# Kernel tuning notes

Measured on AMD Instinct MI355X. Metric: run time of the kernel, lower is better.

## Reference

```python
import jax, jax.numpy as jnp
import numpy as np

D, K, CIN, CD, COUT = 3, 16, 128, 32, 256
C = CIN + CD                  # 160 = C_in + C_delta after concat
DM = -(-COUT // C)            # depth_multiplier = ceil(C_out / C) = 2
N, I = 4, 2048                # batch, points per cloud; M = N*I = 8192


def _bn(x, g, b, eps=1e-5):
    # BatchNorm1d in training mode: biased batch statistics over dim 0
    mu = x.mean(0)
    v = x.var(0)
    return (x - mu) * jax.lax.rsqrt(v + eps) * g + b


def _knn(p, k):
    # knn_graph over ALL M points (wrapper passes no batch vector), loop=True
    d2 = jnp.sum(p * p, axis=1)
    dist = d2[:, None] + d2[None, :] - 2.0 * (p @ p.T)   # [M,M]
    _, idx = jax.lax.top_k(-dist, k)                     # [M,K], self first
    return idx


def _gconv(t, w, b, M):
    # grouped Conv1d(K, K*K, kernel=K, groups=K): t [M,K,K], w [K(cin), K(out/grp), K(tap)]
    return jnp.einsum('mcl,col->mco', t, w).reshape(M, K * K) + b


def _xconv(xf, pf, idx, w1a, b1a, g1a, be1a, w1b, b1b, g1b, be1b,
           w2, b2, g2a, be2a, wc2a, bc2a, g2b, be2b, wc2b, bc2b, g2c, be2c,
           wcd, bcd, wl, bl):
    M = pf.shape[0]
    rel = pf[idx] - pf[:, None, :]                       # [M,K,D] relative neighbor coords
    # mlp1: lift relative coords to C_delta features
    h = rel.reshape(M * K, D)
    h = _bn(jax.nn.elu(h @ w1a + b1a), g1a, be1a)
    h = _bn(jax.nn.elu(h @ w1b + b1b), g1b, be1b)
    x_star = jnp.concatenate([h.reshape(M, K, CD), xf[idx]], axis=-1)  # [M,K,C]
    x_star = x_star.transpose(0, 2, 1)                   # [M,C,K]
    # mlp2: learn KxK X-transformation from the K*D relative coords
    t = _bn(jax.nn.elu(rel.reshape(M, K * D) @ w2 + b2), g2a, be2a).reshape(M, K, K)
    t = _bn(jax.nn.elu(_gconv(t, wc2a, bc2a, M)), g2b, be2b).reshape(M, K, K)
    t = _bn(_gconv(t, wc2b, bc2b, M), g2c, be2c).reshape(M, K, K)
    xt = jnp.einsum('mck,mkj->mcj', x_star, t)           # [M,C,K] batched matmul
    # depthwise Conv1d(C, C*DM, K, groups=C) collapses K, then final Linear
    y = jnp.einsum('mcl,col->mco', xt, wcd).reshape(M, C * DM) + bcd
    return y @ wl + bl                                   # [M,COUT]


def setup_inputs() -> dict:
    key = jax.random.key(0)
    ks = jax.random.split(key, 16)
    r = lambda k, s: jax.random.normal(k, s, jnp.float32) * 0.1
    return dict(
        x=jax.random.normal(ks[0], (N, I, CIN), jnp.float32),
        pos=jax.random.normal(ks[1], (N, I, D), jnp.float32),
        w1a=r(ks[2], (D, CD)), b1a=r(ks[3], (CD,)), g1a=jnp.ones((CD,)), be1a=jnp.zeros((CD,)),
        w1b=r(ks[4], (CD, CD)), b1b=r(ks[5], (CD,)), g1b=jnp.ones((CD,)), be1b=jnp.zeros((CD,)),
        w2=r(ks[6], (D * K, K * K)), b2=r(ks[7], (K * K,)), g2a=jnp.ones((K * K,)), be2a=jnp.zeros((K * K,)),
        wc2a=r(ks[8], (K, K, K)), bc2a=r(ks[9], (K * K,)), g2b=jnp.ones((K * K,)), be2b=jnp.zeros((K * K,)),
        wc2b=r(ks[10], (K, K, K)), bc2b=r(ks[11], (K * K,)), g2c=jnp.ones((K * K,)), be2c=jnp.zeros((K * K,)),
        wcd=r(ks[12], (C, DM, K)), bcd=r(ks[13], (C * DM,)),
        wl=r(ks[14], (C * DM, COUT)), bl=r(ks[15], (COUT,)),
    )


def reference(x, pos, w1a, b1a, g1a, be1a, w1b, b1b, g1b, be1b,
              w2, b2, g2a, be2a, wc2a, bc2a, g2b, be2b, wc2b, bc2b, g2c, be2c,
              wcd, bcd, wl, bl):
    pf = pos.reshape(N * I, D)
    xf = x.reshape(N * I, CIN)
    idx = _knn(pf, K)
    out = _xconv(xf, pf, idx, w1a, b1a, g1a, be1a, w1b, b1b, g1b, be1b,
                 w2, b2, g2a, be2a, wc2a, bc2a, g2b, be2b, wc2b, bc2b, g2c, be2c,
                 wcd, bcd, wl, bl)
    return out.reshape(N, I, COUT)
```

## Files before the change

### kernel.cpp

```cpp
#include <hip/hip_runtime.h>
#include <math.h>

#define M_PTS 8192
#define MK    131072

__device__ __forceinline__ float elu(float v){ return v > 0.f ? v : __expf(v)-1.0f; }

__device__ __forceinline__ unsigned distkey(float4 c, float qx, float qy, float qz, float d2q){
  #pragma clang fp contract(off)
  float dot  = __builtin_fmaf(c.z, qz, __builtin_fmaf(c.y, qy, __builtin_fmaf(c.x, qx, 0.0f)));
  float A    = d2q + c.w;
  float B    = 2.0f * dot;
  float dist = A - B;
  unsigned u = __float_as_uint(dist);
  return u ^ ((unsigned)((int)u >> 31) | 0x80000000u);
}

__global__ __launch_bounds__(256) void knn_kernel(const float* __restrict__ pos,
                                                  int* __restrict__ nidx,
                                                  float* __restrict__ st){
  #pragma clang fp contract(off)
  __shared__ float4 cand[1024];
  __shared__ unsigned long long hits[4][64];
  int tid  = threadIdx.x;
  int lane = tid & 63;
  int wv   = tid >> 6;
  int q    = blockIdx.x*4 + wv;
  if (blockIdx.x == 0){
    for (int i = tid; i < 2048; i += 256) st[i] = 0.f;
  }
  float qx = pos[3*q], qy = pos[3*q+1], qz = pos[3*q+2];
  float d2q = (qx*qx + qy*qy) + qz*qz;

  unsigned ka[8];
  #pragma unroll
  for (int s=0;s<8;s++) ka[s] = 0xFFFFFFFFu;

  for (int base = 0; base < M_PTS; base += 1024){
    for (int t = tid; t < 1024; t += 256){
      int j = base + t;
      float x = pos[3*j], y = pos[3*j+1], z = pos[3*j+2];
      float d2v = (x*x + y*y) + z*z;
      cand[t] = make_float4(x,y,z,d2v);
    }
    __syncthreads();
    #pragma unroll
    for (int k=0; k<16; k++){
      unsigned v = distkey(cand[lane + k*64], qx, qy, qz, d2q);
      #pragma unroll
      for (int s=0;s<8;s++){
        unsigned mn = min(v, ka[s]);
        unsigned mx = max(v, ka[s]);
        ka[s] = mn; v = mx;
      }
    }
    __syncthreads();
  }

  unsigned thr = 0xFFFFFFFFu;
  for (int r=0; r<16; r++){
    unsigned mine = ka[0];
    unsigned best = mine;
    #pragma unroll
    for (int off=32; off>0; off>>=1){
      unsigned o = __shfl_xor(best, off, 64);
      best = min(best, o);
    }
    bool adv = (best == mine);
    #pragma unroll
    for (int s=0;s<7;s++) ka[s] = adv ? ka[s+1] : ka[s];
    ka[7] = adv ? 0xFFFFFFFFu : ka[7];
    thr = best;
  }

  int cnt = 0;
  for (int base = 0; base < M_PTS; base += 1024){
    for (int t = tid; t < 1024; t += 256){
      int j = base + t;
      float x = pos[3*j], y = pos[3*j+1], z = pos[3*j+2];
      float d2v = (x*x + y*y) + z*z;
      cand[t] = make_float4(x,y,z,d2v);
    }
    __syncthreads();
    #pragma unroll
    for (int k=0; k<16; k++){
      int j = base + lane + k*64;
      unsigned u = distkey(cand[lane + k*64], qx, qy, qz, d2q);
      bool hit = (u <= thr);
      unsigned long long m = __ballot(hit);
      if (hit){
        int slot = cnt + __popcll(m & ((1ull<<lane)-1ull));
        if (slot < 64) hits[wv][slot] = ((unsigned long long)u << 32) | (unsigned)j;
      }
      cnt += (int)__popcll(m);
    }
    __syncthreads();
  }

  int cc = min(cnt, 64);
  unsigned long long mine = (lane < cc) ? hits[wv][lane] : ~0ull;
  for (int r=0; r<16; r++){
    unsigned long long best = mine;
    #pragma unroll
    for (int off=32; off>0; off>>=1){
      unsigned long long o = __shfl_xor(best, off, 64);
      best = (o < best) ? o : best;
    }
    if (mine == best) mine = ~0ull;
    if (lane == 0) nidx[q*16 + r] = (int)(unsigned)best;
  }
}

#define COMPUTE_RELF_8()                                              \
  for (int f = tid; f < 8*48; f += 256){                              \
    int p = f/48, kd = f%48, k = kd/3, d = kd%3;                      \
    int j = nidx[(m0+p)*16 + k];                                      \
    relf[p][kd] = pos[3*j+d] - pos[3*(m0+p)+d];                       \
  }                                                                   \
  __syncthreads();

#define COMPUTE_T1_8(acc)                                             \
  _Pragma("unroll")                                                   \
  for (int p=0;p<8;p++) acc[p] = b2[tid];                             \
  for (int kk=0; kk<48; kk++){                                        \
    float w = w2[kk*256 + tid];                                       \
    _Pragma("unroll")                                                 \
    for (int p=0;p<8;p++) acc[p] += relf[p][kk]*w;                    \
  }

__global__ __launch_bounds__(256) void stats_a_kernel(const float* __restrict__ pos,
    const int* __restrict__ nidx,
    const float* __restrict__ w1a, const float* __restrict__ b1a,
    const float* __restrict__ w2,  const float* __restrict__ b2,
    float* __restrict__ tact,
    float* __restrict__ s1, float* __restrict__ s3){
  int tid = threadIdx.x;
  if (blockIdx.x < 512){
    __shared__ float relS[256][3];
    __shared__ float red[8][64];
    int r = blockIdx.x*256 + tid;
    int m = r >> 4;
    int j = nidx[r];
    relS[tid][0] = pos[3*j  ]-pos[3*m  ];
    relS[tid][1] = pos[3*j+1]-pos[3*m+1];
    relS[tid][2] = pos[3*j+2]-pos[3*m+2];
    __syncthreads();
    int c = tid & 31, g = tid >> 5;
    float w0=w1a[c], w1v=w1a[32+c], w2v=w1a[64+c], b=b1a[c];
    float s=0.f, q=0.f;
    for (int rr=g*32; rr<g*32+32; rr++){
      float h = elu(b + relS[rr][0]*w0 + relS[rr][1]*w1v + relS[rr][2]*w2v);
      s += h; q += h*h;
    }
    red[g][c]=s; red[g][32+c]=q;
    __syncthreads();
    if (tid < 64){
      float a=0.f;
      #pragma unroll
      for (int gg=0;gg<8;gg++) a += red[gg][tid];
      atomicAdd(&s1[tid], a);
    }
  } else {
    __shared__ float relf[8][48];
    int m0 = (blockIdx.x-512)*8;
    COMPUTE_RELF_8();
    float acc[8];
    COMPUTE_T1_8(acc);
    float s=0.f, q=0.f;
    #pragma unroll
    for (int p=0;p<8;p++){
      float v = elu(acc[p]);
      s += v; q += v*v;
      tact[(size_t)(m0+p)*256 + tid] = v;
    }
    atomicAdd(&s3[tid], s); atomicAdd(&s3[256+tid], q);
  }
}

__global__ __launch_bounds__(256) void stats_b_kernel(const float* __restrict__ pos,
    const int* __restrict__ nidx,
    const float* __restrict__ w1a, const float* __restrict__ b1a,
    const float* __restrict__ s1,  const float* __restrict__ g1a, const float* __restrict__ be1a,
    const float* __restrict__ w1b, const float* __restrict__ b1b,
    float* __restrict__ tact,
    const float* __restrict__ s3,  const float* __restrict__ g2a, const float* __restrict__ be2a,
    const float* __restrict__ wc2a,const float* __restrict__ bc2a,
    float* __restrict__ s2, float* __restrict__ s4){
  int tid = threadIdx.x;
  const float invMK = 1.f/(float)MK;
  const float invM  = 1.f/8192.f;
  if (blockIdx.x < 2048){
    __shared__ float xnS[64][33];
    __shared__ float red[8][64];
    __shared__ float muA[32], ivA[32];
    if (tid < 32){
      float mu  = s1[tid]*invMK;
      float var = s1[32+tid]*invMK - mu*mu;
      muA[tid] = mu; ivA[tid] = rsqrtf(var+1e-5f)*g1a[tid];
    }
    __syncthreads();
    {
      int rl = tid >> 2;
      int r  = blockIdx.x*64 + rl;
      int m = r >> 4;
      int j = nidx[r];
      float rx = pos[3*j]-pos[3*m], ry = pos[3*j+1]-pos[3*m+1], rz = pos[3*j+2]-pos[3*m+2];
      int c0 = (tid & 3)*8;
      #pragma unroll
      for (int u=0; u<8; u++){
        int cc = c0 + u;
        float h = elu(b1a[cc] + rx*w1a[cc] + ry*w1a[32+cc] + rz*w1a[64+cc]);
        xnS[rl][cc] = (h-muA[cc])*ivA[cc] + be1a[cc];
      }
    }
    __syncthreads();
    int o = tid & 31, g = tid >> 5;
    float wcol[32];
    #pragma unroll
    for (int cc=0;cc<32;cc++) wcol[cc] = w1b[cc*32+o];
    float bo = b1b[o], s=0.f, q=0.f;
    for (int rr=g*8; rr<g*8+8; rr++){
      float a = bo;
      #pragma unroll
      for (int cc=0;cc<32;cc++) a += xnS[rr][cc]*wcol[cc];
      float v = elu(a);
      s += v; q += v*v;
    }
    red[g][o]=s; red[g][32+o]=q;
    __syncthreads();
    if (tid < 64){
      float a=0.f;
      #pragma unroll
      for (int gg=0;gg<8;gg++) a += red[gg][tid];
      atomicAdd(&s2[tid], a);
    }
  } else {
    __shared__ float tn[8][256];
    int m0 = (blockIdx.x-2048)*8;
    float mu3  = s3[tid]*invM;
    float var3 = s3[256+tid]*invM - mu3*mu3;
    float i3   = rsqrtf(var3+1e-5f)*g2a[tid];
    float bb3  = be2a[tid];
    float tv[8];
    #pragma unroll
    for (int p=0;p<8;p++) tv[p] = tact[(size_t)(m0+p)*256 + tid];
    #pragma unroll
    for (int p=0;p<8;p++) tn[p][tid] = (tv[p]-mu3)*i3 + bb3;
    __syncthreads();
    int c = tid >> 4;
    float wreg[16];
    const float4* wv4 = (const float4*)(wc2a + tid*16);
    #pragma unroll
    for (int v=0; v<4; v++){ float4 f = wv4[v]; wreg[4*v]=f.x; wreg[4*v+1]=f.y; wreg[4*v+2]=f.z; wreg[4*v+3]=f.w; }
    float bias = bc2a[tid];
    float s=0.f, q=0.f;
    #pragma unroll
    for (int p=0;p<8;p++){
      float a2 = bias;
      #pragma unroll
      for (int l=0;l<16;l++) a2 += tn[p][c*16+l]*wreg[l];
      float v = elu(a2);
      s += v; q += v*v;
      tv[p] = v;
    }
    #pragma unroll
    for (int p=0;p<8;p++) tact[(size_t)(m0+p)*256 + tid] = tv[p];
    atomicAdd(&s4[tid], s); atomicAdd(&s4[256+tid], q);
  }
}

__global__ __launch_bounds__(256) void t3_stats_kernel(
    float* __restrict__ tact,
    const float* __restrict__ s4, const float* __restrict__ g2b, const float* __restrict__ be2b,
    const float* __restrict__ wc2b, const float* __restrict__ bc2b, float* __restrict__ s5){
  __shared__ float tn2[8][256];
  int m0 = blockIdx.x*8, tid = threadIdx.x;
  const float invM = 1.f/8192.f;
  float mu4  = s4[tid]*invM;
  float var4 = s4[256+tid]*invM - mu4*mu4;
  float i4   = rsqrtf(var4+1e-5f)*g2b[tid];
  float bb4  = be2b[tid];
  float tv[8];
  #pragma unroll
  for (int p=0;p<8;p++) tv[p] = tact[(size_t)(m0+p)*256 + tid];
  #pragma unroll
  for (int p=0;p<8;p++) tn2[p][tid] = (tv[p]-mu4)*i4 + bb4;
  __syncthreads();
  int c = tid >> 4;
  float w2reg[16];
  { const float4* wv4 = (const float4*)(wc2b + tid*16);
    #pragma unroll
    for (int v=0; v<4; v++){ float4 f = wv4[v]; w2reg[4*v]=f.x; w2reg[4*v+1]=f.y; w2reg[4*v+2]=f.z; w2reg[4*v+3]=f.w; } }
  float bias2 = bc2b[tid];
  float s=0.f, q=0.f;
  #pragma unroll
  for (int p=0;p<8;p++){
    float a3 = bias2;
    #pragma unroll
    for (int l=0;l<16;l++) a3 += tn2[p][c*16+l]*w2reg[l];
    s += a3; q += a3*a3;
    tv[p] = a3;
  }
  #pragma unroll
  for (int p=0;p<8;p++) tact[(size_t)(m0+p)*256 + tid] = tv[p];
  atomicAdd(&s5[tid], s); atomicAdd(&s5[256+tid], q);
}

#define PF 4
__global__ __launch_bounds__(256) void final_kernel(
    const float* __restrict__ x, const float* __restrict__ pos, const int* __restrict__ nidx,
    const float* __restrict__ w1a, const float* __restrict__ b1a,
    const float* __restrict__ g1a, const float* __restrict__ be1a,
    const float* __restrict__ w1b, const float* __restrict__ b1b,
    const float* __restrict__ g1b, const float* __restrict__ be1b,
    const float* __restrict__ g2c, const float* __restrict__ be2c,
    const float* __restrict__ wcd, const float* __restrict__ bcd,
    const float* __restrict__ wl,  const float* __restrict__ bl,
    const float* __restrict__ st,
    float* __restrict__ out){
  __shared__ float tA[PF][256];
  __shared__ float xs[PF*32*17];
  __shared__ float yy[PF][320];
  __shared__ int   sidx[PF*16];
  __shared__ float mu1[32], i1g[32], mu2[32], i2g[32];
  int tid = threadIdx.x;
  int m0  = blockIdx.x*PF;
  const float invMK = 1.f/(float)MK;
  const float invM  = 1.f/8192.f;

  if (tid < PF*16) sidx[tid] = nidx[m0*16 + tid];
  if (tid < 32){
    float mu  = st[tid]*invMK;
    float var = st[32+tid]*invMK - mu*mu;
    mu1[tid] = mu; i1g[tid] = rsqrtf(var+1e-5f)*g1a[tid];
    float mu_2  = st[64+tid]*invMK;
    float var_2 = st[96+tid]*invMK - mu_2*mu_2;
    mu2[tid] = mu_2; i2g[tid] = rsqrtf(var_2+1e-5f)*g1b[tid];
  }
  {
    float mu5 = st[1152+tid]*invM, var5 = st[1408+tid]*invM - mu5*mu5;
    float i5 = rsqrtf(var5+1e-5f)*g2c[tid], bb5 = be2c[tid];
    #pragma unroll
    for (int p=0;p<PF;p++){
      float v = out[(size_t)(m0+p)*256 + tid];
      tA[p][tid] = (v-mu5)*i5 + bb5;
    }
  }
  __syncthreads();

  {
    int row = tid >> 2;
    int p = row >> 4, k = row & 15;
    int q8 = (tid & 3)*8;
    int m = m0 + p;
    int j = sidx[p*16 + k];
    float rx = pos[3*j]-pos[3*m], ry = pos[3*j+1]-pos[3*m+1], rz = pos[3*j+2]-pos[3*m+2];
    float xn[32];
    #pragma unroll
    for (int cc=0; cc<32; cc++){
      float h = elu(b1a[cc] + rx*w1a[cc] + ry*w1a[32+cc] + rz*w1a[64+cc]);
      xn[cc] = (h-mu1[cc])*i1g[cc] + be1a[cc];
    }
    #pragma unroll
    for (int oo=0; oo<8; oo++){
      int o = q8 + oo;
      float a = b1b[o];
      #pragma unroll
      for (int cc=0; cc<32; cc++) a += xn[cc]*w1b[cc*32+o];
      float h2v = elu(a);
      xs[(p*32 + o)*17 + k] = (h2v-mu2[o])*i2g[o] + be1b[o];
    }
  }
  __syncthreads();

  for (int pair = tid; pair < PF*160; pair += 256){
    int p = pair / 160, cch = pair % 160;
    float av[16];
    if (cch < 32){
      #pragma unroll
      for (int k16=0;k16<16;k16++) av[k16] = xs[(p*32+cch)*17 + k16];
    } else {
      #pragma unroll
      for (int k16=0;k16<16;k16++) av[k16] = x[(size_t)sidx[p*16+k16]*128 + (cch-32)];
    }
    float xt[16];
    #pragma unroll
    for (int j16=0;j16<16;j16++) xt[j16]=0.f;
    #pragma unroll
    for (int k16=0;k16<16;k16++){
      float a = av[k16];
      #pragma unroll
      for (int j16=0;j16<16;j16++) xt[j16] += a*tA[p][k16*16+j16];
    }
    float y0 = bcd[cch*2], y1 = bcd[cch*2+1];
    #pragma unroll
    for (int l=0;l<16;l++){
      y0 += xt[l]*wcd[cch*32 + l];
      y1 += xt[l]*wcd[cch*32 + 16 + l];
    }
    yy[p][cch*2] = y0; yy[p][cch*2+1] = y1;
  }
  __syncthreads();

  float accO[PF];
  #pragma unroll
  for (int p=0;p<PF;p++) accO[p] = bl[tid];
  for (int q=0;q<320;q++){
    float w = wl[q*256 + tid];
    #pragma unroll
    for (int p=0;p<PF;p++) accO[p] += yy[p][q]*w;
  }
  #pragma unroll
  for (int p=0;p<PF;p++) out[(size_t)(m0+p)*256 + tid] = accO[p];
}

extern "C" void kernel_launch(void* const* d_in, const int* in_sizes, int n_in,
                              void* d_out, int out_size, void* d_ws, size_t ws_size,
                              hipStream_t stream){
  const float* x    = (const float*)d_in[0];
  const float* pos  = (const float*)d_in[1];
  const float* w1a  = (const float*)d_in[2];
  const float* b1a  = (const float*)d_in[3];
  const float* g1a  = (const float*)d_in[4];
  const float* be1a = (const float*)d_in[5];
  const float* w1b  = (const float*)d_in[6];
  const float* b1b  = (const float*)d_in[7];
  const float* g1b  = (const float*)d_in[8];
  const float* be1b = (const float*)d_in[9];
  const float* w2   = (const float*)d_in[10];
  const float* b2   = (const float*)d_in[11];
  const float* g2a  = (const float*)d_in[12];
  const float* be2a = (const float*)d_in[13];
  const float* wc2a = (const float*)d_in[14];
  const float* bc2a = (const float*)d_in[15];
  const float* g2b  = (const float*)d_in[16];
  const float* be2b = (const float*)d_in[17];
  const float* wc2b = (const float*)d_in[18];
  const float* bc2b = (const float*)d_in[19];
  const float* g2c  = (const float*)d_in[20];
  const float* be2c = (const float*)d_in[21];
  const float* wcd  = (const float*)d_in[22];
  const float* bcd  = (const float*)d_in[23];
  const float* wl   = (const float*)d_in[24];
  const float* bl   = (const float*)d_in[25];
  float* out = (float*)d_out;

  char* ws = (char*)d_ws;
  int*   nidx = (int*)(ws + 0);
  float* st   = (float*)(ws + 524288);
  float* s1 = st;
  float* s2 = st + 64;
  float* s3 = st + 128;
  float* s4 = st + 640;
  float* s5 = st + 1152;

  knn_kernel<<<2048,256,0,stream>>>(pos, nidx, st);
  stats_a_kernel<<<1536,256,0,stream>>>(pos, nidx, w1a, b1a, w2, b2, out, s1, s3);
  stats_b_kernel<<<3072,256,0,stream>>>(pos, nidx, w1a, b1a, s1, g1a, be1a, w1b, b1b,
                                        out, s3, g2a, be2a, wc2a, bc2a, s2, s4);
  t3_stats_kernel<<<1024,256,0,stream>>>(out, s4, g2b, be2b, wc2b, bc2b, s5);
  final_kernel<<<2048,256,0,stream>>>(x, pos, nidx,
                                      w1a, b1a, g1a, be1a, w1b, b1b, g1b, be1b,
                                      g2c, be2c, wcd, bcd, wl, bl, st, out);
}
```

Baseline: 392.3 us.

## Use bf16 MFMA for final linear layer and double points per block

```diff
diff --git a/kernel.cpp b/kernel.cpp
--- a/kernel.cpp
+++ b/kernel.cpp
@@ -4,7 +4,20 @@
 #define M_PTS 8192
 #define MK    131072
 
+typedef __attribute__((ext_vector_type(8))) short bf16x8;
+typedef __attribute__((ext_vector_type(4))) float f32x4;
+
 __device__ __forceinline__ float elu(float v){ return v > 0.f ? v : __expf(v)-1.0f; }
+
+__device__ __forceinline__ unsigned cvt_pk_bf16(float lo, float hi){
+  unsigned r;
+  asm("v_cvt_pk_bf16_f32 %0, %1, %2" : "=v"(r) : "v"(lo), "v"(hi));
+  return r;
+}
+__device__ __forceinline__ unsigned short f2bf(float v){
+  unsigned u = __float_as_uint(v);
+  return (unsigned short)((u + 0x7FFFu + ((u>>16)&1u)) >> 16);
+}
 
 __device__ __forceinline__ unsigned distkey(float4 c, float qx, float qy, float qz, float d2q){
   #pragma clang fp contract(off)
@@ -306,7 +319,7 @@
   atomicAdd(&s5[tid], s); atomicAdd(&s5[256+tid], q);
 }
 
-#define PF 4
+#define PF 8
 __global__ __launch_bounds__(256) void final_kernel(
     const float* __restrict__ x, const float* __restrict__ pos, const int* __restrict__ nidx,
     const float* __restrict__ w1a, const float* __restrict__ b1a,
@@ -319,8 +332,8 @@
     const float* __restrict__ st,
     float* __restrict__ out){
   __shared__ float tA[PF][256];
-  __shared__ float xs[PF*32*17];
-  __shared__ float yy[PF][320];
+  __shared__ unsigned short xs[PF*32*17];
+  __shared__ unsigned short yh[16][328];
   __shared__ int   sidx[PF*16];
   __shared__ float mu1[32], i1g[32], mu2[32], i2g[32];
   int tid = threadIdx.x;
@@ -338,6 +351,10 @@
     mu2[tid] = mu_2; i2g[tid] = rsqrtf(var_2+1e-5f)*g1b[tid];
   }
   {
+    unsigned short* yz = &yh[8][0];
+    for (int i = tid; i < 8*328; i += 256) yz[i] = 0;
+  }
+  {
     float mu5 = st[1152+tid]*invM, var5 = st[1408+tid]*invM - mu5*mu5;
     float i5 = rsqrtf(var5+1e-5f)*g2c[tid], bb5 = be2c[tid];
     #pragma unroll
@@ -348,12 +365,12 @@
   }
   __syncthreads();
 
-  {
-    int row = tid >> 2;
-    int p = row >> 4, k = row & 15;
+  for (int half = 0; half < 2; ++half){
+    int row = half*64 + (tid >> 2);
+    int p = row >> 4;
     int q8 = (tid & 3)*8;
     int m = m0 + p;
-    int j = sidx[p*16 + k];
+    int j = sidx[row];
     float rx = pos[3*j]-pos[3*m], ry = pos[3*j+1]-pos[3*m+1], rz = pos[3*j+2]-pos[3*m+2];
     float xn[32];
     #pragma unroll
@@ -361,6 +378,7 @@
       float h = elu(b1a[cc] + rx*w1a[cc] + ry*w1a[32+cc] + rz*w1a[64+cc]);
       xn[cc] = (h-mu1[cc])*i1g[cc] + be1a[cc];
     }
+    int k = row & 15;
     #pragma unroll
     for (int oo=0; oo<8; oo++){
       int o = q8 + oo;
@@ -368,7 +386,7 @@
       #pragma unroll
       for (int cc=0; cc<32; cc++) a += xn[cc]*w1b[cc*32+o];
       float h2v = elu(a);
-      xs[(p*32 + o)*17 + k] = (h2v-mu2[o])*i2g[o] + be1b[o];
+      xs[(p*32 + o)*17 + k] = f2bf((h2v-mu2[o])*i2g[o] + be1b[o]);
     }
   }
   __syncthreads();
@@ -378,7 +396,8 @@
     float av[16];
     if (cch < 32){
       #pragma unroll
-      for (int k16=0;k16<16;k16++) av[k16] = xs[(p*32+cch)*17 + k16];
+      for (int k16=0;k16<16;k16++)
+        av[k16] = __uint_as_float((unsigned)xs[(p*32+cch)*17 + k16] << 16);
     } else {
       #pragma unroll
       for (int k16=0;k16<16;k16++) av[k16] = x[(size_t)sidx[p*16+k16]*128 + (cch-32)];
@@ -398,20 +417,47 @@
       y0 += xt[l]*wcd[cch*32 + l];
       y1 += xt[l]*wcd[cch*32 + 16 + l];
     }
-    yy[p][cch*2] = y0; yy[p][cch*2+1] = y1;
+    *(unsigned*)&yh[p][cch*2] = cvt_pk_bf16(y0, y1);
   }
   __syncthreads();
 
-  float accO[PF];
-  #pragma unroll
-  for (int p=0;p<PF;p++) accO[p] = bl[tid];
-  for (int q=0;q<320;q++){
-    float w = wl[q*256 + tid];
-    #pragma unroll
-    for (int p=0;p<PF;p++) accO[p] += yy[p][q]*w;
-  }
-  #pragma unroll
-  for (int p=0;p<PF;p++) out[(size_t)(m0+p)*256 + tid] = accO[p];
+  {
+    int lane = tid & 63;
+    int wvi  = tid >> 6;
+    int lrow = lane & 15;
+    int lgrp = lane >> 4;
+    int colbase = wvi*64;
+    f32x4 acc[4];
+    #pragma unroll
+    for (int nt=0; nt<4; ++nt) acc[nt] = (f32x4){0.f,0.f,0.f,0.f};
+    for (int kt = 0; kt < 10; ++kt){
+      int k0 = kt*32 + lgrp*8;
+      bf16x8 ah = *(const bf16x8*)&yh[lrow][k0];
+      #pragma unroll
+      for (int nt = 0; nt < 4; ++nt){
+        int col = colbase + nt*16 + lrow;
+        const float* wp = wl + (size_t)k0*256 + col;
+        float w0=wp[0],    w1=wp[256],  w2=wp[512],  w3=wp[768];
+        float w4=wp[1024], w5=wp[1280], w6=wp[1536], w7=wp[1792];
+        union { bf16x8 v; unsigned u[4]; } bu;
+        bu.u[0] = cvt_pk_bf16(w0, w1);
+        bu.u[1] = cvt_pk_bf16(w2, w3);
+        bu.u[2] = cvt_pk_bf16(w4, w5);
+        bu.u[3] = cvt_pk_bf16(w6, w7);
+        acc[nt] = __builtin_amdgcn_mfma_f32_16x16x32_bf16(ah, bu.v, acc[nt], 0, 0, 0);
+      }
+    }
+    #pragma unroll
+    for (int nt=0; nt<4; ++nt){
+      int col = colbase + nt*16 + lrow;
+      float bv = bl[col];
+      #pragma unroll
+      for (int r=0;r<4;r++){
+        int orow = lgrp*4 + r;
+        if (orow < PF) out[(size_t)(m0+orow)*256 + col] = acc[nt][r] + bv;
+      }
+    }
+  }
 }
 
 extern "C" void kernel_launch(void* const* d_in, const int* in_sizes, int n_in,
@@ -459,7 +505,7 @@
   stats_b_kernel<<<3072,256,0,stream>>>(pos, nidx, w1a, b1a, s1, g1a, be1a, w1b, b1b,
                                         out, s3, g2a, be2a, wc2a, bc2a, s2, s4);
   t3_stats_kernel<<<1024,256,0,stream>>>(out, s4, g2b, be2b, wc2b, bc2b, s5);
-  final_kernel<<<2048,256,0,stream>>>(x, pos, nidx,
+  final_kernel<<<1024,256,0,stream>>>(x, pos, nidx,
                                       w1a, b1a, g1a, be1a, w1b, b1b, g1b, be1b,
                                       g2c, be2c, wcd, bcd, wl, bl, st, out);
 }
```

New measurement: 404.0 us. 3.0% more time.

## Split final linear into separate bf16 MFMA GEMM kernel via packed staging

Applied to the files above, without the earlier changes.

```diff
diff --git a/kernel.cpp b/kernel.cpp
--- a/kernel.cpp
+++ b/kernel.cpp
@@ -4,7 +4,16 @@
 #define M_PTS 8192
 #define MK    131072
 
+typedef __attribute__((ext_vector_type(8))) short bf16x8;
+typedef __attribute__((ext_vector_type(4))) float f32x4;
+
 __device__ __forceinline__ float elu(float v){ return v > 0.f ? v : __expf(v)-1.0f; }
+
+__device__ __forceinline__ unsigned cvt_pk_bf16(float lo, float hi){
+  unsigned r;
+  asm("v_cvt_pk_bf16_f32 %0, %1, %2" : "=v"(r) : "v"(lo), "v"(hi));
+  return r;
+}
 
 __device__ __forceinline__ unsigned distkey(float4 c, float qx, float qy, float qz, float d2q){
   #pragma clang fp contract(off)
@@ -315,12 +324,10 @@
     const float* __restrict__ g1b, const float* __restrict__ be1b,
     const float* __restrict__ g2c, const float* __restrict__ be2c,
     const float* __restrict__ wcd, const float* __restrict__ bcd,
-    const float* __restrict__ wl,  const float* __restrict__ bl,
     const float* __restrict__ st,
     float* __restrict__ out){
   __shared__ float tA[PF][256];
   __shared__ float xs[PF*32*17];
-  __shared__ float yy[PF][320];
   __shared__ int   sidx[PF*16];
   __shared__ float mu1[32], i1g[32], mu2[32], i2g[32];
   int tid = threadIdx.x;
@@ -398,20 +405,65 @@
       y0 += xt[l]*wcd[cch*32 + l];
       y1 += xt[l]*wcd[cch*32 + 16 + l];
     }
-    yy[p][cch*2] = y0; yy[p][cch*2+1] = y1;
+    ((unsigned*)out)[(size_t)(m0+p)*256 + cch] = cvt_pk_bf16(y0, y1);
+  }
+}
+
+#define GR 32
+__global__ __launch_bounds__(256) void gemm_final_kernel(
+    const float* __restrict__ wl, const float* __restrict__ bl,
+    float* __restrict__ out){
+  __shared__ unsigned short yh[GR][328];
+  int tid = threadIdx.x;
+  int m0  = blockIdx.x*GR;
+
+  {
+    const uint4* src4 = (const uint4*)out;
+    int r = tid >> 3, seg = tid & 7;
+    #pragma unroll
+    for (int i=0;i<5;i++){
+      uint4 v = src4[(size_t)(m0+r)*64 + seg*5 + i];
+      *(uint4*)&yh[r][(seg*5+i)*8] = v;
+    }
   }
   __syncthreads();
 
-  float accO[PF];
-  #pragma unroll
-  for (int p=0;p<PF;p++) accO[p] = bl[tid];
-  for (int q=0;q<320;q++){
-    float w = wl[q*256 + tid];
-    #pragma unroll
-    for (int p=0;p<PF;p++) accO[p] += yy[p][q]*w;
-  }
-  #pragma unroll
-  for (int p=0;p<PF;p++) out[(size_t)(m0+p)*256 + tid] = accO[p];
+  int lane = tid & 63;
+  int wv   = tid >> 6;
+  int lrow = lane & 15;
+  int lgrp = lane >> 4;
+  int rbase = (wv & 1)*16;
+  int cbase = (wv >> 1)*128;
+  f32x4 acc[8];
+  #pragma unroll
+  for (int nt=0; nt<8; ++nt) acc[nt] = (f32x4){0.f,0.f,0.f,0.f};
+
+  for (int kt = 0; kt < 10; ++kt){
+    int k0 = kt*32 + lgrp*8;
+    bf16x8 ah = *(const bf16x8*)&yh[rbase + lrow][k0];
+    #pragma unroll
+    for (int nt = 0; nt < 8; ++nt){
+      int col = cbase + nt*16 + lrow;
+      const float* wp = wl + (size_t)k0*256 + col;
+      union { bf16x8 v; unsigned u[4]; } bu;
+      bu.u[0] = cvt_pk_bf16(wp[0],    wp[256]);
+      bu.u[1] = cvt_pk_bf16(wp[512],  wp[768]);
+      bu.u[2] = cvt_pk_bf16(wp[1024], wp[1280]);
+      bu.u[3] = cvt_pk_bf16(wp[1536], wp[1792]);
+      acc[nt] = __builtin_amdgcn_mfma_f32_16x16x32_bf16(ah, bu.v, acc[nt], 0, 0, 0);
+    }
+  }
+
+  #pragma unroll
+  for (int nt=0; nt<8; ++nt){
+    int col = cbase + nt*16 + lrow;
+    float bv = bl[col];
+    #pragma unroll
+    for (int r=0;r<4;r++){
+      int orow = rbase + lgrp*4 + r;
+      out[(size_t)(m0+orow)*256 + col] = acc[nt][r] + bv;
+    }
+  }
 }
 
 extern "C" void kernel_launch(void* const* d_in, const int* in_sizes, int n_in,
@@ -461,5 +513,6 @@
   t3_stats_kernel<<<1024,256,0,stream>>>(out, s4, g2b, be2b, wc2b, bc2b, s5);
   final_kernel<<<2048,256,0,stream>>>(x, pos, nidx,
                                       w1a, b1a, g1a, be1a, w1b, b1b, g1b, be1b,
-                                      g2c, be2c, wcd, bcd, wl, bl, st, out);
-}
+                                      g2c, be2c, wcd, bcd, st, out);
+  gemm_final_kernel<<<256,256,0,stream>>>(wl, bl, out);
+}
```

Result: slower. 418.3 us (+6.6%).

## Process two kNN queries per wavefront using packed fp16 sorting network

Applied to the files above, without the earlier changes.

```diff
diff --git a/kernel.cpp b/kernel.cpp
--- a/kernel.cpp
+++ b/kernel.cpp
@@ -4,7 +4,17 @@
 #define M_PTS 8192
 #define MK    131072
 
+typedef __fp16 half2v __attribute__((ext_vector_type(2)));
+union H2U { half2v h; unsigned u; };
+
 __device__ __forceinline__ float elu(float v){ return v > 0.f ? v : __expf(v)-1.0f; }
+
+__device__ __forceinline__ unsigned pk_min_u16(unsigned a, unsigned b){
+  unsigned r; asm("v_pk_min_u16 %0, %1, %2" : "=v"(r) : "v"(a), "v"(b)); return r;
+}
+__device__ __forceinline__ unsigned pk_max_u16(unsigned a, unsigned b){
+  unsigned r; asm("v_pk_max_u16 %0, %1, %2" : "=v"(r) : "v"(a), "v"(b)); return r;
+}
 
 __device__ __forceinline__ unsigned distkey(float4 c, float qx, float qy, float qz, float d2q){
   #pragma clang fp contract(off)
@@ -19,18 +29,24 @@
 __global__ __launch_bounds__(256) void knn_kernel(const float* __restrict__ pos,
                                                   int* __restrict__ nidx,
                                                   float* __restrict__ st){
-  #pragma clang fp contract(off)
   __shared__ float4 cand[1024];
-  __shared__ unsigned long long hits[4][64];
+  __shared__ unsigned long long hits[4][2][64];
   int tid  = threadIdx.x;
   int lane = tid & 63;
   int wv   = tid >> 6;
-  int q    = blockIdx.x*4 + wv;
+  int q0   = blockIdx.x*8 + wv*2;
+  int q1   = q0 + 1;
   if (blockIdx.x == 0){
     for (int i = tid; i < 2048; i += 256) st[i] = 0.f;
   }
-  float qx = pos[3*q], qy = pos[3*q+1], qz = pos[3*q+2];
-  float d2q = (qx*qx + qy*qy) + qz*qz;
+  float qx0 = pos[3*q0], qy0 = pos[3*q0+1], qz0 = pos[3*q0+2];
+  float qx1 = pos[3*q1], qy1 = pos[3*q1+1], qz1 = pos[3*q1+2];
+  float d2q0, d2q1;
+  {
+    #pragma clang fp contract(off)
+    d2q0 = (qx0*qx0 + qy0*qy0) + qz0*qz0;
+    d2q1 = (qx1*qx1 + qy1*qy1) + qz1*qz1;
+  }
 
   unsigned ka[8];
   #pragma unroll
@@ -38,6 +54,7 @@
 
   for (int base = 0; base < M_PTS; base += 1024){
     for (int t = tid; t < 1024; t += 256){
+      #pragma clang fp contract(off)
       int j = base + t;
       float x = pos[3*j], y = pos[3*j+1], z = pos[3*j+2];
       float d2v = (x*x + y*y) + z*z;
@@ -46,36 +63,56 @@
     __syncthreads();
     #pragma unroll
     for (int k=0; k<16; k++){
-      unsigned v = distkey(cand[lane + k*64], qx, qy, qz, d2q);
+      float4 c = cand[lane + k*64];
+      float dot0 = c.x*qx0 + c.y*qy0 + c.z*qz0;
+      float dot1 = c.x*qx1 + c.y*qy1 + c.z*qz1;
+      float d0 = fmaxf((d2q0 + c.w) - 2.0f*dot0, 0.f);
+      float d1 = fmaxf((d2q1 + c.w) - 2.0f*dot1, 0.f);
+      H2U pu; pu.h = __builtin_amdgcn_cvt_pkrtz(d0, d1);
+      unsigned v = pu.u;
       #pragma unroll
       for (int s=0;s<8;s++){
-        unsigned mn = min(v, ka[s]);
-        unsigned mx = max(v, ka[s]);
+        unsigned mn = pk_min_u16(v, ka[s]);
+        unsigned mx = pk_max_u16(v, ka[s]);
         ka[s] = mn; v = mx;
       }
     }
     __syncthreads();
   }
 
-  unsigned thr = 0xFFFFFFFFu;
-  for (int r=0; r<16; r++){
-    unsigned mine = ka[0];
-    unsigned best = mine;
-    #pragma unroll
-    for (int off=32; off>0; off>>=1){
-      unsigned o = __shfl_xor(best, off, 64);
-      best = min(best, o);
-    }
-    bool adv = (best == mine);
-    #pragma unroll
-    for (int s=0;s<7;s++) ka[s] = adv ? ka[s+1] : ka[s];
-    ka[7] = adv ? 0xFFFFFFFFu : ka[7];
-    thr = best;
-  }
-
-  int cnt = 0;
+  unsigned thr16[2];
+  #pragma unroll
+  for (int qq=0; qq<2; qq++){
+    unsigned kq[8];
+    #pragma unroll
+    for (int s=0;s<8;s++) kq[s] = (qq==0) ? (ka[s] & 0xFFFFu) : (ka[s] >> 16);
+    unsigned t16 = 0xFFFFu;
+    for (int r=0; r<16; r++){
+      unsigned mine = kq[0];
+      unsigned best = mine;
+      #pragma unroll
+      for (int off=32; off>0; off>>=1){
+        unsigned o = __shfl_xor(best, off, 64);
+        best = min(best, o);
+      }
+      bool adv = (best == mine);
+      #pragma unroll
+      for (int s=0;s<7;s++) kq[s] = adv ? kq[s+1] : kq[s];
+      kq[7] = adv ? 0xFFFFu : kq[7];
+      t16 = best;
+    }
+    thr16[qq] = t16;
+  }
+  unsigned t0u = min(thr16[0] + 2u, 0x7C00u);
+  unsigned t1u = min(thr16[1] + 2u, 0x7C00u);
+  float thrF0, thrF1;
+  asm("v_cvt_f32_f16 %0, %1" : "=v"(thrF0) : "v"(t0u));
+  asm("v_cvt_f32_f16 %0, %1" : "=v"(thrF1) : "v"(t1u));
+
+  int cnt0 = 0, cnt1 = 0;
   for (int base = 0; base < M_PTS; base += 1024){
     for (int t = tid; t < 1024; t += 256){
+      #pragma clang fp contract(off)
       int j = base + t;
       float x = pos[3*j], y = pos[3*j+1], z = pos[3*j+2];
       float d2v = (x*x + y*y) + z*z;
@@ -85,29 +122,48 @@
     #pragma unroll
     for (int k=0; k<16; k++){
       int j = base + lane + k*64;
-      unsigned u = distkey(cand[lane + k*64], qx, qy, qz, d2q);
-      bool hit = (u <= thr);
-      unsigned long long m = __ballot(hit);
-      if (hit){
-        int slot = cnt + __popcll(m & ((1ull<<lane)-1ull));
-        if (slot < 64) hits[wv][slot] = ((unsigned long long)u << 32) | (unsigned)j;
+      float4 c = cand[lane + k*64];
+      float dot0 = c.x*qx0 + c.y*qy0 + c.z*qz0;
+      float dot1 = c.x*qx1 + c.y*qy1 + c.z*qz1;
+      bool h0 = ((d2q0 + c.w) - 2.0f*dot0) <= thrF0;
+      bool h1 = ((d2q1 + c.w) - 2.0f*dot1) <= thrF1;
+      unsigned long long m0 = __ballot(h0);
+      unsigned long long m1 = __ballot(h1);
+      if (m0){
+        unsigned u = distkey(c, qx0, qy0, qz0, d2q0);
+        if (h0){
+          int slot = cnt0 + __popcll(m0 & ((1ull<<lane)-1ull));
+          if (slot < 64) hits[wv][0][slot] = ((unsigned long long)u << 32) | (unsigned)j;
+        }
+        cnt0 += (int)__popcll(m0);
       }
-      cnt += (int)__popcll(m);
-    }
-    __syncthreads();
-  }
-
-  int cc = min(cnt, 64);
-  unsigned long long mine = (lane < cc) ? hits[wv][lane] : ~0ull;
-  for (int r=0; r<16; r++){
-    unsigned long long best = mine;
-    #pragma unroll
-    for (int off=32; off>0; off>>=1){
-      unsigned long long o = __shfl_xor(best, off, 64);
-      best = (o < best) ? o : best;
-    }
-    if (mine == best) mine = ~0ull;
-    if (lane == 0) nidx[q*16 + r] = (int)(unsigned)best;
+      if (m1){
+        unsigned u = distkey(c, qx1, qy1, qz1, d2q1);
+        if (h1){
+          int slot = cnt1 + __popcll(m1 & ((1ull<<lane)-1ull));
+          if (slot < 64) hits[wv][1][slot] = ((unsigned long long)u << 32) | (unsigned)j;
+        }
+        cnt1 += (int)__popcll(m1);
+      }
+    }
+    __syncthreads();
+  }
+
+  #pragma unroll
+  for (int qq=0; qq<2; qq++){
+    int cc = min(qq == 0 ? cnt0 : cnt1, 64);
+    int qo = (qq == 0 ? q0 : q1)*16;
+    unsigned long long mine = (lane < cc) ? hits[wv][qq][lane] : ~0ull;
+    for (int r=0; r<16; r++){
+      unsigned long long best = mine;
+      #pragma unroll
+      for (int off=32; off>0; off>>=1){
+        unsigned long long o = __shfl_xor(best, off, 64);
+        best = (o < best) ? o : best;
+      }
+      if (mine == best) mine = ~0ull;
+      if (lane == 0) nidx[qo + r] = (int)(unsigned)best;
+    }
   }
 }
 
@@ -454,7 +510,7 @@
   float* s4 = st + 640;
   float* s5 = st + 1152;
 
-  knn_kernel<<<2048,256,0,stream>>>(pos, nidx, st);
+  knn_kernel<<<1024,256,0,stream>>>(pos, nidx, st);
   stats_a_kernel<<<1536,256,0,stream>>>(pos, nidx, w1a, b1a, w2, b2, out, s1, s3);
   stats_b_kernel<<<3072,256,0,stream>>>(pos, nidx, w1a, b1a, s1, g1a, be1a, w1b, b1b,
                                         out, s3, g2a, be2a, wc2a, bc2a, s2, s4);
```

After: 391.2 us. Within noise of the previous version (-0.3%).
